# Kernel tuning notes

Measured on AMD Instinct MI355X. Metric: run time of the kernel, lower is better.

Reference implementation:

```python
import jax, jax.numpy as jnp
import numpy as np

ALPHA = 0.2  # LeakyReLU negative slope


def setup_inputs() -> dict:
    key = jax.random.key(0)
    k1, k2 = jax.random.split(key)
    B, N, Fin, Fout = 4, 4096, 256, 128
    h = jax.random.normal(k1, (B, N, Fin), dtype=jnp.float32)
    adj = jnp.zeros((B, N, N), dtype=bool)  # unused by the original forward
    # Linear(in,out,bias=False); stored as [in,out] for h @ W
    W = jax.random.normal(k2, (Fin, Fout), dtype=jnp.float32) * (1.0 / np.sqrt(Fin))
    return {"h": h, "adj": adj, "W": W}


def reference(h, adj, W):
    # h: [B,N,Fin], W: [Fin,Fout]
    hp = jnp.einsum("bnf,fo->bno", h, W)                    # [B,N,Fout]
    e = jnp.einsum("bnd,bmd->bnm", hp, hp)                  # [B,N,N]
    e = jnp.where(e >= 0, e, ALPHA * e)                      # LeakyReLU
    attn = jax.nn.softmax(e, axis=1)                         # softmax over dim=1 (rows)
    # torch: sum_j( hp[b,i] * attn[b,i,j] ) == hp[b,i] * sum_j attn[b,i,j]
    row_mass = jnp.sum(attn, axis=2, keepdims=True)          # [B,N,1]
    return hp * row_mass
```

## Files before the change

kernel.cpp:

```cpp
#include <hip/hip_runtime.h>
#include <hip/hip_bf16.h>

#define ALPHA 0.2f

constexpr int BN   = 4;
constexpr int NN   = 4096;
constexpr int FIN  = 256;
constexpr int FOUT = 128;
constexpr int NT   = 64;
constexpr int NPAIR = NT * (NT + 1) / 2;

typedef __attribute__((ext_vector_type(8))) short bf16x8;
typedef __attribute__((ext_vector_type(4))) float f32x4;

#define MFMA16(a, b, c) __builtin_amdgcn_mfma_f32_16x16x32_bf16((a), (b), (c), 0, 0, 0)

template<int CTRL>
__device__ __forceinline__ float dpp_mov(float x) {
    return __int_as_float(__builtin_amdgcn_update_dpp(
        __float_as_int(x), __float_as_int(x), CTRL, 0xF, 0xF, false));
}
__device__ __forceinline__ float rsum16(float x) {
    x += dpp_mov<0x128>(x);
    x += dpp_mov<0x124>(x);
    x += dpp_mov<0x122>(x);
    x += dpp_mov<0x121>(x);
    return x;
}
__device__ __forceinline__ float rmax16(float x) {
    x = fmaxf(x, dpp_mov<0x128>(x));
    x = fmaxf(x, dpp_mov<0x124>(x));
    x = fmaxf(x, dpp_mov<0x122>(x));
    x = fmaxf(x, dpp_mov<0x121>(x));
    return x;
}

__device__ __forceinline__ void split8(const float* x, uint4& H, uint4& L) {
    ushort hb[8], lb[8];
    #pragma unroll
    for (int i = 0; i < 8; ++i) {
        float xv = x[i];
        __hip_bfloat16 hh = __float2bfloat16(xv);
        float hf = __bfloat162float(hh);
        __hip_bfloat16 lw = __float2bfloat16(xv - hf);
        hb[i] = reinterpret_cast<const ushort&>(hh);
        lb[i] = reinterpret_cast<const ushort&>(lw);
    }
    H = make_uint4((uint)hb[0] | ((uint)hb[1] << 16), (uint)hb[2] | ((uint)hb[3] << 16),
                   (uint)hb[4] | ((uint)hb[5] << 16), (uint)hb[6] | ((uint)hb[7] << 16));
    L = make_uint4((uint)lb[0] | ((uint)lb[1] << 16), (uint)lb[2] | ((uint)lb[3] << 16),
                   (uint)lb[4] | ((uint)lb[5] << 16), (uint)lb[6] | ((uint)lb[7] << 16));
}

template<int ROWS, int KGSH>
__device__ __forceinline__ void stage_split(const float* __restrict__ src, int strideF,
                                            ushort* hi, ushort* lo, int tid) {
    constexpr int KG = 1 << KGSH;
    #pragma unroll
    for (int idx = tid; idx < ROWS * KG; idx += 256) {
        int row = idx >> KGSH, g = idx & (KG - 1);
        const float4* p4 = reinterpret_cast<const float4*>(src + (size_t)row * strideF + g * 8);
        float4 u = p4[0], v = p4[1];
        float x[8] = {u.x, u.y, u.z, u.w, v.x, v.y, v.z, v.w};
        uint4 H, L;
        split8(x, H, L);
        int gran = (row << KGSH) + (g ^ (row & 7));
        reinterpret_cast<uint4*>(hi)[gran] = H;
        reinterpret_cast<uint4*>(lo)[gran] = L;
    }
}
template<int ROWS, int KGSH>
__device__ __forceinline__ void stage_copy(const ushort* __restrict__ src, int strideU,
                                           ushort* dst, int tid) {
    constexpr int KG = 1 << KGSH;
    #pragma unroll
    for (int idx = tid; idx < ROWS * KG; idx += 256) {
        int row = idx >> KGSH, g = idx & (KG - 1);
        uint4 vv = *reinterpret_cast<const uint4*>(src + (size_t)row * strideU + g * 8);
        reinterpret_cast<uint4*>(dst)[(row << KGSH) + (g ^ (row & 7))] = vv;
    }
}
__device__ __forceinline__ bf16x8 frag16(const ushort* s, int rowbase, int kstep, int kgsh, int lane) {
    int r = rowbase + (lane & 15);
    int g = kstep * 4 + (lane >> 4);
    int gran = (r << kgsh) + (g ^ (r & 7));
    return *reinterpret_cast<const bf16x8*>(s + gran * 8);
}

__global__ void k_prepW(const float* __restrict__ W, ushort* __restrict__ Wt_hi,
                        ushort* __restrict__ Wt_lo) {
    int idx = blockIdx.x * 256 + threadIdx.x;
    if (idx >= FOUT * (FIN / 8)) return;
    int n = idx >> 5, g = idx & 31;
    float x[8];
    #pragma unroll
    for (int i = 0; i < 8; ++i) x[i] = W[(size_t)(g * 8 + i) * FOUT + n];
    uint4 H, L;
    split8(x, H, L);
    reinterpret_cast<uint4*>(Wt_hi)[n * 32 + g] = H;
    reinterpret_cast<uint4*>(Wt_lo)[n * 32 + g] = L;
}

__global__ __launch_bounds__(256)
void k_hp(const float* __restrict__ h, const ushort* __restrict__ Wt_hi,
          const ushort* __restrict__ Wt_lo, float* __restrict__ hp,
          ushort* __restrict__ hp_hi, ushort* __restrict__ hp_lo) {
    __shared__ __align__(16) ushort Ah[64 * 64], Al[64 * 64];
    __shared__ __align__(16) ushort Bh[128 * 64], Bl[128 * 64];
    const int tid = threadIdx.x, lane = tid & 63, wid = tid >> 6;
    const int wy = wid >> 1, wx = wid & 1;
    const int ibase = blockIdx.x * 64;
    f32x4 z = {0.f, 0.f, 0.f, 0.f};
    f32x4 acc[2][4] = {{z, z, z, z}, {z, z, z, z}};
    for (int kt = 0; kt < 4; ++kt) {
        __syncthreads();
        stage_split<64, 3>(h + (size_t)ibase * FIN + kt * 64, FIN, Ah, Al, tid);
        stage_copy<128, 3>(Wt_hi + kt * 64, FIN, Bh, tid);
        stage_copy<128, 3>(Wt_lo + kt * 64, FIN, Bl, tid);
        __syncthreads();
        #pragma unroll
        for (int pr = 0; pr < 3; ++pr) {
            const ushort* A = (pr == 2) ? Al : Ah;
            const ushort* B = (pr == 1) ? Bl : Bh;
            #pragma unroll
            for (int ks = 0; ks < 2; ++ks) {
                bf16x8 a0 = frag16(A, wy * 32, ks, 3, lane);
                bf16x8 a1 = frag16(A, wy * 32 + 16, ks, 3, lane);
                #pragma unroll
                for (int c = 0; c < 4; ++c) {
                    bf16x8 bb = frag16(B, wx * 64 + c * 16, ks, 3, lane);
                    acc[0][c] = MFMA16(a0, bb, acc[0][c]);
                    acc[1][c] = MFMA16(a1, bb, acc[1][c]);
                }
            }
        }
    }
    #pragma unroll
    for (int r = 0; r < 2; ++r)
        #pragma unroll
        for (int c = 0; c < 4; ++c)
            #pragma unroll
            for (int p = 0; p < 4; ++p) {
                int row = ibase + wy * 32 + r * 16 + (lane >> 4) * 4 + p;
                int col = wx * 64 + c * 16 + (lane & 15);
                float x = acc[r][c][p];
                __hip_bfloat16 hh = __float2bfloat16(x);
                float hf = __bfloat162float(hh);
                __hip_bfloat16 lw = __float2bfloat16(x - hf);
                size_t off = (size_t)row * FOUT + col;
                hp[off] = x;
                hp_hi[off] = reinterpret_cast<const ushort&>(hh);
                hp_lo[off] = reinterpret_cast<const ushort&>(lw);
            }
}

__device__ __forceinline__ void decode_task(int task, int& b, int& ti, int& tj) {
    b = task / NPAIR;
    int sub = task - b * NPAIR;
    int t = 0, width = NT;
    while (sub >= width) { sub -= width; --width; ++t; }
    ti = t;
    tj = t + sub;
}

__device__ __forceinline__ void etile_g(const ushort* __restrict__ Hh,
                                        const ushort* __restrict__ Hl,
                                        int ibase, int jbase, int lane,
                                        f32x4 acc[4][4]) {
    const int lrow = lane & 15, lg = lane >> 4;
    #pragma unroll
    for (int ks = 0; ks < 4; ++ks) {
        const int g8 = (ks * 4 + lg) * 8;
        bf16x8 aH[4], aL[4];
        #pragma unroll
        for (int r = 0; r < 4; ++r) {
            size_t off = (size_t)(ibase + r * 16 + lrow) * FOUT + g8;
            aH[r] = *reinterpret_cast<const bf16x8*>(Hh + off);
            aL[r] = *reinterpret_cast<const bf16x8*>(Hl + off);
        }
        #pragma unroll
        for (int c = 0; c < 4; ++c) {
            size_t off = (size_t)(jbase + c * 16 + lrow) * FOUT + g8;
            bf16x8 bH = *reinterpret_cast<const bf16x8*>(Hh + off);
            bf16x8 bL = *reinterpret_cast<const bf16x8*>(Hl + off);
            #pragma unroll
            for (int r = 0; r < 4; ++r) {
                acc[r][c] = MFMA16(aH[r], bH, acc[r][c]);
                acc[r][c] = MFMA16(aH[r], bL, acc[r][c]);
                acc[r][c] = MFMA16(aL[r], bH, acc[r][c]);
            }
        }
    }
}

__global__ __launch_bounds__(256)
void k_stats(const ushort* __restrict__ hp_hi, const ushort* __restrict__ hp_lo,
             float* __restrict__ m_part, float* __restrict__ s_part) {
    const int tid = threadIdx.x, lane = tid & 63, wid = tid >> 6;
    const int lrow = lane & 15, lg = lane >> 4;
    int b, ti, tj;
    decode_task(blockIdx.x * 4 + wid, b, ti, tj);
    const size_t bo = (size_t)b * NN * FOUT;
    const int ibase = ti * 64, jbase = tj * 64;
    f32x4 z = {0.f, 0.f, 0.f, 0.f};
    f32x4 acc[4][4] = {{z,z,z,z},{z,z,z,z},{z,z,z,z},{z,z,z,z}};
    etile_g(hp_hi + bo, hp_lo + bo, ibase, jbase, lane, acc);
    #pragma unroll
    for (int r = 0; r < 4; ++r)
        #pragma unroll
        for (int c = 0; c < 4; ++c)
            #pragma unroll
            for (int p = 0; p < 4; ++p) {
                float x = acc[r][c][p];
                acc[r][c][p] = fmaxf(x, ALPHA * x);
            }
    {
        float* mp = m_part + (size_t)(b * NT + tj) * NN;
        float* sp = s_part + (size_t)(b * NT + tj) * NN;
        #pragma unroll
        for (int r = 0; r < 4; ++r)
            #pragma unroll
            for (int p = 0; p < 4; ++p) {
                float mx = fmaxf(fmaxf(acc[r][0][p], acc[r][1][p]),
                                 fmaxf(acc[r][2][p], acc[r][3][p]));
                mx = rmax16(mx);
                float se = 0.f;
                #pragma unroll
                for (int c = 0; c < 4; ++c) se += __expf(acc[r][c][p] - mx);
                se = rsum16(se);
                if (lrow == 0) {
                    int i = ibase + r * 16 + lg * 4 + p;
                    mp[i] = mx;
                    sp[i] = se;
                }
            }
    }
    if (ti != tj) {
        float* mp = m_part + (size_t)(b * NT + ti) * NN;
        float* sp = s_part + (size_t)(b * NT + ti) * NN;
        #pragma unroll
        for (int c = 0; c < 4; ++c) {
            float mx = -1e30f;
            #pragma unroll
            for (int r = 0; r < 4; ++r)
                #pragma unroll
                for (int p = 0; p < 4; ++p) mx = fmaxf(mx, acc[r][c][p]);
            mx = fmaxf(mx, __shfl_xor(mx, 16));
            mx = fmaxf(mx, __shfl_xor(mx, 32));
            float se = 0.f;
            #pragma unroll
            for (int r = 0; r < 4; ++r)
                #pragma unroll
                for (int p = 0; p < 4; ++p) se += __expf(acc[r][c][p] - mx);
            se += __shfl_xor(se, 16);
            se += __shfl_xor(se, 32);
            if (lane < 16) {
                int j = jbase + c * 16 + lane;
                mp[j] = mx;
                sp[j] = se;
            }
        }
    }
}

__global__ void k_merge(const float* __restrict__ m_part, const float* __restrict__ s_part,
                        float* __restrict__ m_fin, float* __restrict__ inv_s) {
    int idx = blockIdx.x * 256 + threadIdx.x;
    if (idx >= BN * NN) return;
    int b = idx >> 12, row = idx & (NN - 1);
    const float* mp = m_part + (size_t)b * NT * NN + row;
    const float* sp = s_part + (size_t)b * NT * NN + row;
    float M = -1e30f;
    for (int k = 0; k < NT; ++k) M = fmaxf(M, mp[(size_t)k * NN]);
    float S = 0.f;
    for (int k = 0; k < NT; ++k) S += sp[(size_t)k * NN] * __expf(mp[(size_t)k * NN] - M);
    m_fin[idx] = M;
    inv_s[idx] = 1.f / S;
}

__global__ __launch_bounds__(256)
void k_mass(const ushort* __restrict__ hp_hi, const ushort* __restrict__ hp_lo,
            const float* __restrict__ m_fin, const float* __restrict__ inv_s,
            float* __restrict__ rs_part) {
    const int tid = threadIdx.x, lane = tid & 63, wid = tid >> 6;
    const int lrow = lane & 15, lg = lane >> 4;
    int b, ti, tj;
    decode_task(blockIdx.x * 4 + wid, b, ti, tj);
    const size_t bo = (size_t)b * NN * FOUT;
    const int ibase = ti * 64, jbase = tj * 64;
    f32x4 z = {0.f, 0.f, 0.f, 0.f};
    f32x4 acc[4][4] = {{z,z,z,z},{z,z,z,z},{z,z,z,z},{z,z,z,z}};
    etile_g(hp_hi + bo, hp_lo + bo, ibase, jbase, lane, acc);
    const float* mf = m_fin + (size_t)b * NN;
    const float* isv = inv_s + (size_t)b * NN;
    float mj[4], sj[4];
    #pragma unroll
    for (int c = 0; c < 4; ++c) {
        int j = jbase + c * 16 + lrow;
        mj[c] = mf[j];
        sj[c] = isv[j];
    }
    {
        float* rs = rs_part + (size_t)(b * NT + tj) * NN;
        #pragma unroll
        for (int r = 0; r < 4; ++r)
            #pragma unroll
            for (int p = 0; p < 4; ++p) {
                float s = 0.f;
                #pragma unroll
                for (int c = 0; c < 4; ++c) {
                    float x = acc[r][c][p];
                    float g = fmaxf(x, ALPHA * x);
                    s += __expf(g - mj[c]) * sj[c];
                }
                s = rsum16(s);
                if (lrow == 0) rs[ibase + r * 16 + lg * 4 + p] = s;
            }
    }
    if (ti != tj) {
        float mi[4][4], si_[4][4];
        #pragma unroll
        for (int r = 0; r < 4; ++r)
            #pragma unroll
            for (int p = 0; p < 4; ++p) {
                int i = ibase + r * 16 + lg * 4 + p;
                mi[r][p] = mf[i];
                si_[r][p] = isv[i];
            }
        float* rs = rs_part + (size_t)(b * NT + ti) * NN;
        #pragma unroll
        for (int c = 0; c < 4; ++c) {
            float s2 = 0.f;
            #pragma unroll
            for (int r = 0; r < 4; ++r)
                #pragma unroll
                for (int p = 0; p < 4; ++p) {
                    float x = acc[r][c][p];
                    float g = fmaxf(x, ALPHA * x);
                    s2 += __expf(g - mi[r][p]) * si_[r][p];
                }
            s2 += __shfl_xor(s2, 16);
            s2 += __shfl_xor(s2, 32);
            if (lane < 16) rs[jbase + c * 16 + lane] = s2;
        }
    }
}

__global__ void k_scale(const float* __restrict__ rs_part, float* __restrict__ out) {
    int idx = blockIdx.x * 256 + threadIdx.x;
    if (idx >= BN * NN * FOUT / 4) return;
    int row = idx >> 5;
    int b = row >> 12, i = row & (NN - 1);
    const float* rs = rs_part + (size_t)b * NT * NN + i;
    float rm = 0.f;
    for (int k = 0; k < NT; ++k) rm += rs[(size_t)k * NN];
    float4 v = reinterpret_cast<float4*>(out)[idx];
    v.x *= rm; v.y *= rm; v.z *= rm; v.w *= rm;
    reinterpret_cast<float4*>(out)[idx] = v;
}

extern "C" void kernel_launch(void* const* d_in, const int* in_sizes, int n_in,
                              void* d_out, int out_size, void* d_ws, size_t ws_size,
                              hipStream_t stream) {
    (void)in_sizes; (void)n_in; (void)out_size; (void)ws_size;
    const float* h = (const float*)d_in[0];
    const float* W = (const float*)d_in[2];
    float* out = (float*)d_out;
    ushort* hp_hi = (ushort*)d_ws;
    ushort* hp_lo = hp_hi + (size_t)BN * NN * FOUT;
    ushort* Wt_hi = hp_lo + (size_t)BN * NN * FOUT;
    ushort* Wt_lo = Wt_hi + FOUT * FIN;
    float* m_part = (float*)(Wt_lo + FOUT * FIN);
    float* s_part = m_part + (size_t)BN * NT * NN;
    float* m_fin  = s_part + (size_t)BN * NT * NN;
    float* inv_s  = m_fin + (size_t)BN * NN;
    float* rs_part = inv_s + (size_t)BN * NN;

    k_prepW<<<(FOUT * (FIN / 8) + 255) / 256, 256, 0, stream>>>(W, Wt_hi, Wt_lo);
    k_hp<<<BN * NN / 64, 256, 0, stream>>>(h, Wt_hi, Wt_lo, out, hp_hi, hp_lo);
    k_stats<<<BN * NPAIR / 4, 256, 0, stream>>>(hp_hi, hp_lo, m_part, s_part);
    k_merge<<<(BN * NN + 255) / 256, 256, 0, stream>>>(m_part, s_part, m_fin, inv_s);
    k_mass<<<BN * NPAIR / 4, 256, 0, stream>>>(hp_hi, hp_lo, m_fin, inv_s, rs_part);
    k_scale<<<(BN * NN * FOUT / 4 + 255) / 256, 256, 0, stream>>>(rs_part, out);
}
```

Baseline: 503.8 us.

## Pre-pack hp hi/lo splits into MFMA fragment order and interleave batch tasks

Adds a separate pack kernel that writes the bf16 hi/lo halves of hp in the exact per-lane MFMA fragment layout, so the E-tile loads in the stats and mass kernels become fully contiguous 16-byte-per-lane reads instead of strided row gathers. The hp kernel now stores only the fp32 result. Block-to-task mapping is changed to interleave batches across consecutive blocks, and launch bounds request 3 blocks per CU for occupancy. This costs an extra kernel launch and an extra read of hp in exchange for coalesced loads in the two dominant kernels.

```diff
diff --git a/kernel.cpp b/kernel.cpp
--- a/kernel.cpp
+++ b/kernel.cpp
@@ -103,8 +103,7 @@
 
 __global__ __launch_bounds__(256)
 void k_hp(const float* __restrict__ h, const ushort* __restrict__ Wt_hi,
-          const ushort* __restrict__ Wt_lo, float* __restrict__ hp,
-          ushort* __restrict__ hp_hi, ushort* __restrict__ hp_lo) {
+          const ushort* __restrict__ Wt_lo, float* __restrict__ hp) {
     __shared__ __align__(16) ushort Ah[64 * 64], Al[64 * 64];
     __shared__ __align__(16) ushort Bh[128 * 64], Bl[128 * 64];
     const int tid = threadIdx.x, lane = tid & 63, wid = tid >> 6;
@@ -143,46 +142,54 @@
             for (int p = 0; p < 4; ++p) {
                 int row = ibase + wy * 32 + r * 16 + (lane >> 4) * 4 + p;
                 int col = wx * 64 + c * 16 + (lane & 15);
-                float x = acc[r][c][p];
-                __hip_bfloat16 hh = __float2bfloat16(x);
-                float hf = __bfloat162float(hh);
-                __hip_bfloat16 lw = __float2bfloat16(x - hf);
-                size_t off = (size_t)row * FOUT + col;
-                hp[off] = x;
-                hp_hi[off] = reinterpret_cast<const ushort&>(hh);
-                hp_lo[off] = reinterpret_cast<const ushort&>(lw);
-            }
-}
-
-__device__ __forceinline__ void decode_task(int task, int& b, int& ti, int& tj) {
-    b = task / NPAIR;
-    int sub = task - b * NPAIR;
+                hp[(size_t)row * FOUT + col] = acc[r][c][p];
+            }
+}
+
+__global__ void k_fragpack(const float* __restrict__ hp, ushort* __restrict__ hi,
+                           ushort* __restrict__ lo) {
+    int t = blockIdx.x * 256 + threadIdx.x;
+    int l = t & 63, ks = (t >> 6) & 3, P = (t >> 8) & 255, b = t >> 16;
+    int row = P * 16 + (l & 15), c8 = ks * 4 + (l >> 4);
+    const float* src = hp + ((size_t)b * NN + row) * FOUT + c8 * 8;
+    const float4* p4 = reinterpret_cast<const float4*>(src);
+    float4 u = p4[0], v = p4[1];
+    float x[8] = {u.x, u.y, u.z, u.w, v.x, v.y, v.z, v.w};
+    uint4 H, L;
+    split8(x, H, L);
+    size_t o = (((size_t)b * 256 + P) * 4 + ks) * 64 + l;
+    reinterpret_cast<uint4*>(hi)[o] = H;
+    reinterpret_cast<uint4*>(lo)[o] = L;
+}
+
+__device__ __forceinline__ void decode2(int bid, int wid, int& b, int& ti, int& tj) {
+    int slot = bid & 7;
+    b = slot >> 1;
+    int sub = ((bid >> 3) << 1) | (slot & 1);
+    int tb = sub * 4 + wid;
     int t = 0, width = NT;
-    while (sub >= width) { sub -= width; --width; ++t; }
+    while (tb >= width) { tb -= width; --width; ++t; }
     ti = t;
-    tj = t + sub;
-}
-
-__device__ __forceinline__ void etile_g(const ushort* __restrict__ Hh,
-                                        const ushort* __restrict__ Hl,
-                                        int ibase, int jbase, int lane,
-                                        f32x4 acc[4][4]) {
-    const int lrow = lane & 15, lg = lane >> 4;
+    tj = t + tb;
+}
+
+__device__ __forceinline__ void etile_fl(const uint4* __restrict__ H4,
+                                         const uint4* __restrict__ L4,
+                                         int pi, int pj, int lane, f32x4 acc[4][4]) {
     #pragma unroll
     for (int ks = 0; ks < 4; ++ks) {
-        const int g8 = (ks * 4 + lg) * 8;
         bf16x8 aH[4], aL[4];
         #pragma unroll
         for (int r = 0; r < 4; ++r) {
-            size_t off = (size_t)(ibase + r * 16 + lrow) * FOUT + g8;
-            aH[r] = *reinterpret_cast<const bf16x8*>(Hh + off);
-            aL[r] = *reinterpret_cast<const bf16x8*>(Hl + off);
+            size_t idx = ((size_t)(pi + r) * 4 + ks) * 64 + lane;
+            aH[r] = *reinterpret_cast<const bf16x8*>(&H4[idx]);
+            aL[r] = *reinterpret_cast<const bf16x8*>(&L4[idx]);
         }
         #pragma unroll
         for (int c = 0; c < 4; ++c) {
-            size_t off = (size_t)(jbase + c * 16 + lrow) * FOUT + g8;
-            bf16x8 bH = *reinterpret_cast<const bf16x8*>(Hh + off);
-            bf16x8 bL = *reinterpret_cast<const bf16x8*>(Hl + off);
+            size_t jdx = ((size_t)(pj + c) * 4 + ks) * 64 + lane;
+            bf16x8 bH = *reinterpret_cast<const bf16x8*>(&H4[jdx]);
+            bf16x8 bL = *reinterpret_cast<const bf16x8*>(&L4[jdx]);
             #pragma unroll
             for (int r = 0; r < 4; ++r) {
                 acc[r][c] = MFMA16(aH[r], bH, acc[r][c]);
@@ -193,18 +200,19 @@
     }
 }
 
-__global__ __launch_bounds__(256)
+__global__ __launch_bounds__(256, 3)
 void k_stats(const ushort* __restrict__ hp_hi, const ushort* __restrict__ hp_lo,
              float* __restrict__ m_part, float* __restrict__ s_part) {
     const int tid = threadIdx.x, lane = tid & 63, wid = tid >> 6;
     const int lrow = lane & 15, lg = lane >> 4;
     int b, ti, tj;
-    decode_task(blockIdx.x * 4 + wid, b, ti, tj);
-    const size_t bo = (size_t)b * NN * FOUT;
+    decode2(blockIdx.x, wid, b, ti, tj);
+    const uint4* H4 = reinterpret_cast<const uint4*>(hp_hi) + (size_t)b * 256 * 256;
+    const uint4* L4 = reinterpret_cast<const uint4*>(hp_lo) + (size_t)b * 256 * 256;
     const int ibase = ti * 64, jbase = tj * 64;
     f32x4 z = {0.f, 0.f, 0.f, 0.f};
     f32x4 acc[4][4] = {{z,z,z,z},{z,z,z,z},{z,z,z,z},{z,z,z,z}};
-    etile_g(hp_hi + bo, hp_lo + bo, ibase, jbase, lane, acc);
+    etile_fl(H4, L4, ti * 4, tj * 4, lane, acc);
     #pragma unroll
     for (int r = 0; r < 4; ++r)
         #pragma unroll
@@ -278,19 +286,20 @@
     inv_s[idx] = 1.f / S;
 }
 
-__global__ __launch_bounds__(256)
+__global__ __launch_bounds__(256, 3)
 void k_mass(const ushort* __restrict__ hp_hi, const ushort* __restrict__ hp_lo,
             const float* __restrict__ m_fin, const float* __restrict__ inv_s,
             float* __restrict__ rs_part) {
     const int tid = threadIdx.x, lane = tid & 63, wid = tid >> 6;
     const int lrow = lane & 15, lg = lane >> 4;
     int b, ti, tj;
-    decode_task(blockIdx.x * 4 + wid, b, ti, tj);
-    const size_t bo = (size_t)b * NN * FOUT;
+    decode2(blockIdx.x, wid, b, ti, tj);
+    const uint4* H4 = reinterpret_cast<const uint4*>(hp_hi) + (size_t)b * 256 * 256;
+    const uint4* L4 = reinterpret_cast<const uint4*>(hp_lo) + (size_t)b * 256 * 256;
     const int ibase = ti * 64, jbase = tj * 64;
     f32x4 z = {0.f, 0.f, 0.f, 0.f};
     f32x4 acc[4][4] = {{z,z,z,z},{z,z,z,z},{z,z,z,z},{z,z,z,z}};
-    etile_g(hp_hi + bo, hp_lo + bo, ibase, jbase, lane, acc);
+    etile_fl(H4, L4, ti * 4, tj * 4, lane, acc);
     const float* mf = m_fin + (size_t)b * NN;
     const float* isv = inv_s + (size_t)b * NN;
     float mj[4], sj[4];
@@ -377,7 +386,8 @@
     float* rs_part = inv_s + (size_t)BN * NN;
 
     k_prepW<<<(FOUT * (FIN / 8) + 255) / 256, 256, 0, stream>>>(W, Wt_hi, Wt_lo);
-    k_hp<<<BN * NN / 64, 256, 0, stream>>>(h, Wt_hi, Wt_lo, out, hp_hi, hp_lo);
+    k_hp<<<BN * NN / 64, 256, 0, stream>>>(h, Wt_hi, Wt_lo, out);
+    k_fragpack<<<BN * 256 * 4 * 64 / 256, 256, 0, stream>>>(out, hp_hi, hp_lo);
     k_stats<<<BN * NPAIR / 4, 256, 0, stream>>>(hp_hi, hp_lo, m_part, s_part);
     k_merge<<<(BN * NN + 255) / 256, 256, 0, stream>>>(m_part, s_part, m_fin, inv_s);
     k_mass<<<BN * NPAIR / 4, 256, 0, stream>>>(hp_hi, hp_lo, m_fin, inv_s, rs_part);
```

Result: faster. 418.6 us (-16.9%).
